# Kernel tuning notes

Measured on AMD Instinct MI355X. Metric: run time of the kernel, lower is better.

## Reference

```python
import jax, jax.numpy as jnp
import numpy as np

NUM_HEADS = 12


def _rel_indices(H, W):
    # [N, N, 3] with channels (dx, dy, dx^2+dy^2), N = H*W
    indx = jnp.arange(W)[None, :] - jnp.arange(W)[:, None]          # [W, W]
    indx = jnp.tile(indx, (H, H))                                    # [N, N]
    indy = jnp.arange(H)[None, :] - jnp.arange(H)[:, None]          # [H, H]
    indy = jnp.repeat(jnp.repeat(indy, W, axis=0), W, axis=1)        # [N, N]
    indd = indx ** 2 + indy ** 2
    return jnp.stack([indx, indy, indd], axis=-1).astype(jnp.float32)


def setup_inputs() -> dict:
    key = jax.random.key(0)
    ks = jax.random.split(key, 8)
    B, N, C = 16, 576, 768
    std = 0.02
    return {
        "x": jax.random.normal(ks[0], (B, N, C), dtype=jnp.float32),
        "Wq": jax.random.normal(ks[1], (C, C), dtype=jnp.float32) * std,
        "Wk": jax.random.normal(ks[2], (C, C), dtype=jnp.float32) * std,
        "Wv": jax.random.normal(ks[3], (C, C), dtype=jnp.float32) * std,
        "Wproj": jax.random.normal(ks[4], (C, C), dtype=jnp.float32) * std,
        "bproj": jnp.zeros((C,), dtype=jnp.float32),
        "pos_w": jax.random.normal(ks[5], (3, NUM_HEADS), dtype=jnp.float32) * std,
        "pos_b": jnp.zeros((NUM_HEADS,), dtype=jnp.float32),
        "gating": jnp.ones((NUM_HEADS,), dtype=jnp.float32),
        "H": 24,
        "W": 24,
    }


def reference(x, Wq, Wk, Wv, Wproj, bproj, pos_w, pos_b, gating, H, W):
    B, N, C = x.shape
    h = gating.shape[0]
    d = C // h
    scale = d ** (-0.5)

    def heads(t):  # [B,N,C] -> [B,h,N,d]
        return t.reshape(B, N, h, d).transpose(0, 2, 1, 3)

    q = heads(x @ Wq)
    k = heads(x @ Wk)
    v = heads(x @ Wv)

    # content scores: [B,h,N,N]
    patch_score = jax.nn.softmax(jnp.einsum('bhnd,bhmd->bhnm', q, k) * scale, axis=-1)

    # positional scores: shared across batch, [h,N,N]
    rel = _rel_indices(H, W)                      # [N,N,3]
    pos_score = jnp.einsum('nmc,ch->hnm', rel, pos_w) + pos_b[:, None, None]
    pos_score = jax.nn.softmax(pos_score, axis=-1)

    gate = jax.nn.sigmoid(gating)[None, :, None, None]  # [1,h,1,1]
    attn = (1.0 - gate) * patch_score + gate * pos_score[None]
    attn = attn / jnp.sum(attn, axis=-1, keepdims=True)

    out = jnp.einsum('bhnm,bhmd->bhnd', attn, v)         # [B,h,N,d]
    out = out.transpose(0, 2, 1, 3).reshape(B, N, C)
    return out @ Wproj + bproj
```

## Files before the change

### kernel.cpp

```cpp
#include <hip/hip_runtime.h>
#include <math.h>

#define B_ 16
#define N_ 576
#define C_ 768
#define NH 12
#define D_ 64
#define GW 24
#define STR 68
#define QKV 2304

typedef unsigned short u16;
typedef __bf16 bf16x8 __attribute__((ext_vector_type(8)));
typedef float f32x4 __attribute__((ext_vector_type(4)));

__device__ __forceinline__ u16 f2bf(float f) {
    unsigned u = __builtin_bit_cast(unsigned, f);
    unsigned r = (u + 0x7FFFu + ((u >> 16) & 1u)) >> 16;
    return (u16)r;
}
__device__ __forceinline__ float bf2f(u16 b) {
    unsigned u = ((unsigned)b) << 16;
    return __builtin_bit_cast(float, u);
}

__device__ __forceinline__ bf16x8 ldsF8u(const u16* p) {
    union { uint2 u[2]; bf16x8 v; } t;
    t.u[0] = *(const uint2*)p;
    t.u[1] = *(const uint2*)(p + 4);
    return t.v;
}
__device__ __forceinline__ bf16x8 ldsF8a(const u16* p) {
    union { uint4 u; bf16x8 v; } t;
    t.u = *(const uint4*)p;
    return t.v;
}

__device__ __forceinline__ void gload16(const u16* g, u16* l) {
    __builtin_amdgcn_global_load_lds(
        (const __attribute__((address_space(1))) void*)g,
        (__attribute__((address_space(3))) void*)l,
        16, 0, 0);
}

__global__ __launch_bounds__(256)
void prep_kernel(const float* __restrict__ x,
                 const float* __restrict__ w0, const float* __restrict__ w1,
                 const float* __restrict__ w2, const float* __restrict__ w3,
                 u16* __restrict__ xb, u16* __restrict__ wt_base)
{
    const int tid = threadIdx.x;
    if (blockIdx.z == 4) {
        const int flat = blockIdx.y * 24 + blockIdx.x;
#pragma unroll
        for (int it = 0; it < 12; ++it) {
            int idx = flat * 3072 + it * 256 + tid;
            float4 v = ((const float4*)x)[idx];
            u16 o[4] = {f2bf(v.x), f2bf(v.y), f2bf(v.z), f2bf(v.w)};
            *(uint2*)&xb[(size_t)idx * 4] = *(const uint2*)o;
        }
        return;
    }
    const float* srcs[4] = {w0, w1, w2, w3};
    const float* src = srcs[blockIdx.z];
    u16* dst = wt_base + (size_t)blockIdx.z * C_ * C_;
    __shared__ float t[32][33];
    const int bx = blockIdx.x * 32, by = blockIdx.y * 32;
    const int tx = tid & 31, ty = tid >> 5;
#pragma unroll
    for (int i = 0; i < 32; i += 8)
        t[ty + i][tx] = src[(size_t)(by + ty + i) * C_ + bx + tx];
    __syncthreads();
#pragma unroll
    for (int i = 0; i < 32; i += 8)
        dst[(size_t)(bx + ty + i) * C_ + by + tx] = f2bf(t[tx][ty + i]);
}

__global__ __launch_bounds__(256)
void mfma_gemm(const u16* __restrict__ A,
               const u16* __restrict__ BT,
               const float* __restrict__ bias,
               float* __restrict__ out,
               u16* __restrict__ outb,
               int ldo, int mode)
{
    const int K = C_;
    __shared__ __align__(16) u16 As[64 * 64];
    __shared__ __align__(16) u16 Bs[128 * 64];
    const int tid = threadIdx.x;
    const int wave = tid >> 6, lane = tid & 63;
    const int quad = lane >> 4, l16 = lane & 15;
    const int wy = wave >> 1, wx = wave & 1;
    const int tm = blockIdx.y * 64, tn = blockIdx.x * 128;

    const int lr = lane >> 3;
    const int sc = ((lane & 7) ^ lr) * 8;

    f32x4 acc[2][4];
#pragma unroll
    for (int i = 0; i < 2; ++i)
#pragma unroll
        for (int j = 0; j < 4; ++j)
            acc[i][j] = (f32x4){0.f, 0.f, 0.f, 0.f};

    for (int k0 = 0; k0 < K; k0 += 64) {
        __syncthreads();
#pragma unroll
        for (int t = 0; t < 2; ++t) {
            const int rg = wave * 16 + t * 8;
            gload16(A + (size_t)(tm + rg + lr) * K + k0 + sc, &As[rg * 64]);
        }
#pragma unroll
        for (int t = 0; t < 4; ++t) {
            const int rg = wave * 32 + t * 8;
            gload16(BT + (size_t)(tn + rg + lr) * K + k0 + sc, &Bs[rg * 64]);
        }
        __syncthreads();

#pragma unroll
        for (int kh = 0; kh < 2; ++kh) {
            const int s = (kh * 4 + quad) ^ (l16 & 7);
            bf16x8 aA[2], bB[4];
#pragma unroll
            for (int i = 0; i < 2; ++i)
                aA[i] = ldsF8a(&As[(wy * 32 + i * 16 + l16) * 64 + s * 8]);
#pragma unroll
            for (int j = 0; j < 4; ++j)
                bB[j] = ldsF8a(&Bs[(wx * 64 + j * 16 + l16) * 64 + s * 8]);
#pragma unroll
            for (int i = 0; i < 2; ++i)
#pragma unroll
                for (int j = 0; j < 4; ++j)
                    acc[i][j] = __builtin_amdgcn_mfma_f32_16x16x32_bf16(aA[i], bB[j], acc[i][j], 0, 0, 0);
        }
    }

    if (mode == 0) {
#pragma unroll
        for (int i = 0; i < 2; ++i) {
#pragma unroll
            for (int r = 0; r < 4; ++r) {
                const int m = tm + wy * 32 + i * 16 + quad * 4 + r;
#pragma unroll
                for (int j = 0; j < 4; ++j) {
                    const int c = tn + wx * 64 + j * 16 + l16;
                    out[(size_t)m * ldo + c] = acc[i][j][r] + bias[c];
                }
            }
        }
    } else {
        const float scale = (tn < C_) ? 0.125f : 1.0f;
#pragma unroll
        for (int i = 0; i < 2; ++i) {
#pragma unroll
            for (int r = 0; r < 4; ++r) {
                const int m = tm + wy * 32 + i * 16 + quad * 4 + r;
#pragma unroll
                for (int j = 0; j < 4; ++j) {
                    const int c = tn + wx * 64 + j * 16 + l16;
                    outb[(size_t)m * ldo + c] = f2bf(acc[i][j][r] * scale);
                }
            }
        }
    }
}

__global__ __launch_bounds__(256)
void tv_pos1_kernel(const u16* __restrict__ qkvb,
                    const float* __restrict__ pos_w,
                    u16* __restrict__ vtb,
                    float* __restrict__ T1)
{
    const int bh = blockIdx.y;
    const int b = bh / NH, h = bh % NH;
    const int tid = threadIdx.x;

    if (blockIdx.x < 9) {
        __shared__ u16 t[64 * 72];
        const int n0 = blockIdx.x * 64;
        const u16* src = qkvb + ((size_t)b * N_ + n0) * QKV + 2 * C_ + h * D_;
#pragma unroll
        for (int p = 0; p < 2; ++p) {
            int idx = p * 256 + tid;
            int r = idx >> 3, c = (idx & 7) << 3;
            *(uint4*)&t[r * 72 + c] = *(const uint4*)(src + (size_t)r * QKV + c);
        }
        __syncthreads();
        u16* dst = vtb + (size_t)bh * D_ * N_ + n0;
#pragma unroll
        for (int p = 0; p < 2; ++p) {
            int idx = p * 256 + tid;
            int dd = idx >> 3, n8 = (idx & 7) << 3;
            u16 o[8];
#pragma unroll
            for (int j = 0; j < 8; ++j) o[j] = t[(n8 + j) * 72 + dd];
            *(uint4*)(dst + (size_t)dd * N_ + n8) = *(const uint4*)o;
        }
        return;
    }

    __shared__ float ey[47];
    const float w1 = pos_w[NH + h], w2 = pos_w[2 * NH + h];
    if (tid < 47) {
        float dy = (float)(tid - 23);
        ey[tid] = __expf(w1 * dy + w2 * dy * dy);
    }
    __syncthreads();
    if (tid >= 192) return;
    const int mx = tid >> 3, c = (tid & 7) << 3;
    const u16* src = qkvb + (size_t)b * N_ * QKV + 2 * C_ + h * D_ + c;

#pragma unroll
    for (int np = 0; np < 3; ++np) {
        float acc[8][8];
#pragma unroll
        for (int q = 0; q < 8; ++q)
#pragma unroll
            for (int j = 0; j < 8; ++j) acc[q][j] = 0.f;
        for (int my = 0; my < GW; ++my) {
            union { uint4 u; u16 s[8]; } d;
            d.u = *(const uint4*)(src + (size_t)(my * GW + mx) * QKV);
            float vf[8];
#pragma unroll
            for (int j = 0; j < 8; ++j) vf[j] = bf2f(d.s[j]);
#pragma unroll
            for (int q = 0; q < 8; ++q) {
                float e = ey[my - (np * 8 + q) + 23];
#pragma unroll
                for (int j = 0; j < 8; ++j) acc[q][j] += e * vf[j];
            }
        }
#pragma unroll
        for (int q = 0; q < 8; ++q) {
            const int ny = np * 8 + q;
            float* dst = T1 + (((size_t)bh * GW + ny) * GW + mx) * D_ + c;
            *(float4*)dst       = *(float4*)&acc[q][0];
            *(float4*)(dst + 4) = *(float4*)&acc[q][4];
        }
    }
}

__global__ __launch_bounds__(256)
void pos_stage2_kernel(const float* __restrict__ T1,
                       const float* __restrict__ pos_w,
                       const float* __restrict__ gating,
                       u16* __restrict__ aob)
{
    const int bh = blockIdx.x;
    const int ny = blockIdx.y;
    const int b = bh / NH, h = bh % NH;
    const int tid = threadIdx.x;
    __shared__ float T1s[GW * D_];
    __shared__ float ex[47];
    __shared__ float SxA[GW];
    __shared__ float Sy;
    const float w0 = pos_w[h], w1 = pos_w[NH + h], w2 = pos_w[2 * NH + h];

    const float* tsrc = T1 + ((size_t)bh * GW + ny) * GW * D_;
#pragma unroll
    for (int i = 0; i < 2; ++i) {
        int idx = i * 256 + tid;
        if (idx < 384) ((float4*)T1s)[idx] = ((const float4*)tsrc)[idx];
    }
    if (tid < 47) {
        float dx = (float)(tid - 23);
        ex[tid] = __expf(w0 * dx + w2 * dx * dx);
    }
    if (tid == 192) {
        float s = 0.f;
        for (int my = 0; my < GW; ++my) {
            float dy = (float)(my - ny);
            s += __expf(w1 * dy + w2 * dy * dy);
        }
        Sy = s;
    }
    __syncthreads();
    if (tid < GW) {
        float s = 0.f;
        for (int mx = 0; mx < GW; ++mx) s += ex[mx - tid + 23];
        SxA[tid] = s;
    }
    __syncthreads();
    if (tid >= 192) return;
    const int nx = tid >> 3, c = (tid & 7) << 3;

    float acc[8];
#pragma unroll
    for (int j = 0; j < 8; ++j) acc[j] = 0.f;
    for (int mx = 0; mx < GW; ++mx) {
        float e = ex[mx - nx + 23];
        float4 t0 = *(float4*)&T1s[mx * D_ + c];
        float4 t1 = *(float4*)&T1s[mx * D_ + c + 4];
        acc[0] += e * t0.x; acc[1] += e * t0.y; acc[2] += e * t0.z; acc[3] += e * t0.w;
        acc[4] += e * t1.x; acc[5] += e * t1.y; acc[6] += e * t1.z; acc[7] += e * t1.w;
    }
    const float g = 1.f / (1.f + __expf(-gating[h]));
    const float sc = g / (SxA[nx] * Sy);
    const int n = ny * GW + nx;
    u16* dst = aob + ((size_t)b * N_ + n) * C_ + h * D_ + c;
    u16 cur[8];
    *(uint4*)cur = *(const uint4*)dst;
    u16 o[8];
#pragma unroll
    for (int j = 0; j < 8; ++j) o[j] = f2bf(bf2f(cur[j]) + sc * acc[j]);
    *(uint4*)dst = *(const uint4*)o;
}

__global__ __launch_bounds__(256)
void attn_kernel(const u16* __restrict__ qkvb,
                 const u16* __restrict__ vt,
                 const float* __restrict__ gating,
                 u16* __restrict__ ao)
{
    const int qt = blockIdx.x;
    const int bh = blockIdx.y;
    const int b = bh / NH, h = bh % NH;
    const int tid = threadIdx.x;
    const int wave = tid >> 6, lane = tid & 63;
    const int quad = lane >> 4, l16 = lane & 15;

    __shared__ u16 smem[3 * 64 * STR];
    u16* Kt = smem;
    u16* Vs = smem + 64 * STR;
    u16* Pb = smem + 2 * 64 * STR;

    const u16* qptr  = qkvb + ((size_t)b * N_ + qt * 64) * QKV + h * D_;
    const u16* kbase = qkvb + (size_t)b * N_ * QKV + C_ + h * D_;
    const u16* vbase = vt + (size_t)bh * D_ * N_;

    const int sr = tid >> 3;
    const int scol = (tid & 7) << 3;

#pragma unroll
    for (int p = 0; p < 2; ++p) {
        int r = p * 32 + sr;
        uint4 d = *(const uint4*)(qptr + (size_t)r * QKV + scol);
        *(uint2*)&Pb[r * STR + scol]     = make_uint2(d.x, d.y);
        *(uint2*)&Pb[r * STR + scol + 4] = make_uint2(d.z, d.w);
    }
    __syncthreads();

    const int arow = wave * 16 + l16;
    bf16x8 aq0 = ldsF8u(&Pb[arow * STR + quad * 8]);
    bf16x8 aq1 = ldsF8u(&Pb[arow * STR + 32 + quad * 8]);

    uint4 rk[2], rv[2];
    auto loadT = [&](int m0) {
#pragma unroll
        for (int p = 0; p < 2; ++p) {
            int r = p * 32 + sr;
            rk[p] = *(const uint4*)(kbase + (size_t)(m0 + r) * QKV + scol);
            rv[p] = *(const uint4*)(vbase + (size_t)r * N_ + m0 + scol);
        }
    };
    auto writeT = [&]() {
#pragma unroll
        for (int p = 0; p < 2; ++p) {
            int r = p * 32 + sr;
            *(uint2*)&Kt[r * STR + scol]     = make_uint2(rk[p].x, rk[p].y);
            *(uint2*)&Kt[r * STR + scol + 4] = make_uint2(rk[p].z, rk[p].w);
            *(uint2*)&Vs[r * STR + scol]     = make_uint2(rv[p].x, rv[p].y);
            *(uint2*)&Vs[r * STR + scol + 4] = make_uint2(rv[p].z, rv[p].w);
        }
    };

    loadT(0);

    f32x4 oc[4];
#pragma unroll
    for (int nt = 0; nt < 4; ++nt)
        oc[nt] = (f32x4){0.f, 0.f, 0.f, 0.f};
    float lrun[4] = {0.f, 0.f, 0.f, 0.f};

    for (int mt = 0; mt < 9; ++mt) {
        __syncthreads();
        writeT();
        __syncthreads();
        if (mt < 8) loadT((mt + 1) * 64);

        f32x4 s[4];
#pragma unroll
        for (int nt = 0; nt < 4; ++nt) {
            bf16x8 b0 = ldsF8u(&Kt[(nt * 16 + l16) * STR + quad * 8]);
            bf16x8 b1 = ldsF8u(&Kt[(nt * 16 + l16) * STR + 32 + quad * 8]);
            f32x4 z = (f32x4){0.f, 0.f, 0.f, 0.f};
            z = __builtin_amdgcn_mfma_f32_16x16x32_bf16(aq0, b0, z, 0, 0, 0);
            z = __builtin_amdgcn_mfma_f32_16x16x32_bf16(aq1, b1, z, 0, 0, 0);
            s[nt] = z;
        }

#pragma unroll
        for (int r = 0; r < 4; ++r) {
            const int prow = (wave * 16 + quad * 4 + r) * STR;
            float e0 = __expf(s[0][r]);
            float e1 = __expf(s[1][r]);
            float e2 = __expf(s[2][r]);
            float e3 = __expf(s[3][r]);
            Pb[prow +  0 + l16] = f2bf(e0);
            Pb[prow + 16 + l16] = f2bf(e1);
            Pb[prow + 32 + l16] = f2bf(e2);
            Pb[prow + 48 + l16] = f2bf(e3);
            lrun[r] += (e0 + e1) + (e2 + e3);
        }
        asm volatile("s_waitcnt lgkmcnt(0)" ::: "memory");

#pragma unroll
        for (int ks = 0; ks < 2; ++ks) {
            bf16x8 ap = ldsF8u(&Pb[arow * STR + ks * 32 + quad * 8]);
#pragma unroll
            for (int nt = 0; nt < 4; ++nt) {
                bf16x8 bv = ldsF8u(&Vs[(nt * 16 + l16) * STR + ks * 32 + quad * 8]);
                oc[nt] = __builtin_amdgcn_mfma_f32_16x16x32_bf16(ap, bv, oc[nt], 0, 0, 0);
            }
        }
    }

#pragma unroll
    for (int r = 0; r < 4; ++r) {
        lrun[r] += __shfl_xor(lrun[r], 1, 64);
        lrun[r] += __shfl_xor(lrun[r], 2, 64);
        lrun[r] += __shfl_xor(lrun[r], 4, 64);
        lrun[r] += __shfl_xor(lrun[r], 8, 64);
    }

    const float g = 1.f / (1.f + __expf(-gating[h]));
#pragma unroll
    for (int r = 0; r < 4; ++r) {
        const float sc = (1.f - g) / lrun[r];
        const int row = qt * 64 + wave * 16 + quad * 4 + r;
#pragma unroll
        for (int nt = 0; nt < 4; ++nt) {
            ao[((size_t)b * N_ + row) * C_ + h * D_ + nt * 16 + l16] =
                f2bf(oc[nt][r] * sc);
        }
    }
}

extern "C" void kernel_launch(void* const* d_in, const int* in_sizes, int n_in,
                              void* d_out, int out_size, void* d_ws, size_t ws_size,
                              hipStream_t stream)
{
    const float* x      = (const float*)d_in[0];
    const float* Wq     = (const float*)d_in[1];
    const float* Wk     = (const float*)d_in[2];
    const float* Wv     = (const float*)d_in[3];
    const float* Wproj  = (const float*)d_in[4];
    const float* bproj  = (const float*)d_in[5];
    const float* pos_w  = (const float*)d_in[6];
    const float* gating = (const float*)d_in[8];
    float* out = (float*)d_out;

    const size_t xe = (size_t)B_ * N_ * C_;
    const size_t we = (size_t)C_ * C_;
    const size_t qe = (size_t)B_ * N_ * QKV;
    u16* xb   = (u16*)d_ws;
    u16* wt   = xb + xe;
    u16* qkvb = wt + 4 * we;
    u16* vtb  = qkvb + qe;
    u16* aob  = vtb + xe;
    float* T1 = (float*)(aob + xe);
    size_t need = (size_t)(3 * xe + 4 * we + qe) * sizeof(u16)
                + (size_t)B_ * NH * GW * GW * D_ * sizeof(float);
    if (ws_size < need) return;

    prep_kernel<<<dim3(24, 24, 5), 256, 0, stream>>>(x, Wq, Wk, Wv, Wproj, xb, wt);

    mfma_gemm<<<dim3(18, 144), 256, 0, stream>>>(xb, wt, nullptr, nullptr,
                                                 qkvb, QKV, 1);
    tv_pos1_kernel<<<dim3(10, B_ * NH), 256, 0, stream>>>(qkvb, pos_w, vtb, T1);
    attn_kernel<<<dim3(9, B_ * NH), 256, 0, stream>>>(qkvb, vtb, gating, aob);
    pos_stage2_kernel<<<dim3(B_ * NH, GW), 256, 0, stream>>>(T1, pos_w, gating, aob);
    mfma_gemm<<<dim3(6, 144), 256, 0, stream>>>(aob, wt + 3 * we, bproj, out,
                                                nullptr, C_, 0);
}
```

Measured before the change: 261.0 us.

## Fuse V transpose into QKV GEMM epilogue and pos stage1 into attention

```diff
diff --git a/kernel.cpp b/kernel.cpp
--- a/kernel.cpp
+++ b/kernel.cpp
@@ -82,6 +82,7 @@
                const float* __restrict__ bias,
                float* __restrict__ out,
                u16* __restrict__ outb,
+               u16* __restrict__ vtb,
                int ldo, int mode)
 {
     const int K = C_;
@@ -162,80 +163,22 @@
                 }
             }
         }
-    }
-}
-
-__global__ __launch_bounds__(256)
-void tv_pos1_kernel(const u16* __restrict__ qkvb,
-                    const float* __restrict__ pos_w,
-                    u16* __restrict__ vtb,
-                    float* __restrict__ T1)
-{
-    const int bh = blockIdx.y;
-    const int b = bh / NH, h = bh % NH;
-    const int tid = threadIdx.x;
-
-    if (blockIdx.x < 9) {
-        __shared__ u16 t[64 * 72];
-        const int n0 = blockIdx.x * 64;
-        const u16* src = qkvb + ((size_t)b * N_ + n0) * QKV + 2 * C_ + h * D_;
-#pragma unroll
-        for (int p = 0; p < 2; ++p) {
-            int idx = p * 256 + tid;
-            int r = idx >> 3, c = (idx & 7) << 3;
-            *(uint4*)&t[r * 72 + c] = *(const uint4*)(src + (size_t)r * QKV + c);
-        }
-        __syncthreads();
-        u16* dst = vtb + (size_t)bh * D_ * N_ + n0;
-#pragma unroll
-        for (int p = 0; p < 2; ++p) {
-            int idx = p * 256 + tid;
-            int dd = idx >> 3, n8 = (idx & 7) << 3;
-            u16 o[8];
-#pragma unroll
-            for (int j = 0; j < 8; ++j) o[j] = t[(n8 + j) * 72 + dd];
-            *(uint4*)(dst + (size_t)dd * N_ + n8) = *(const uint4*)o;
-        }
-        return;
-    }
-
-    __shared__ float ey[47];
-    const float w1 = pos_w[NH + h], w2 = pos_w[2 * NH + h];
-    if (tid < 47) {
-        float dy = (float)(tid - 23);
-        ey[tid] = __expf(w1 * dy + w2 * dy * dy);
-    }
-    __syncthreads();
-    if (tid >= 192) return;
-    const int mx = tid >> 3, c = (tid & 7) << 3;
-    const u16* src = qkvb + (size_t)b * N_ * QKV + 2 * C_ + h * D_ + c;
-
-#pragma unroll
-    for (int np = 0; np < 3; ++np) {
-        float acc[8][8];
-#pragma unroll
-        for (int q = 0; q < 8; ++q)
-#pragma unroll
-            for (int j = 0; j < 8; ++j) acc[q][j] = 0.f;
-        for (int my = 0; my < GW; ++my) {
-            union { uint4 u; u16 s[8]; } d;
-            d.u = *(const uint4*)(src + (size_t)(my * GW + mx) * QKV);
-            float vf[8];
-#pragma unroll
-            for (int j = 0; j < 8; ++j) vf[j] = bf2f(d.s[j]);
-#pragma unroll
-            for (int q = 0; q < 8; ++q) {
-                float e = ey[my - (np * 8 + q) + 23];
-#pragma unroll
-                for (int j = 0; j < 8; ++j) acc[q][j] += e * vf[j];
-            }
-        }
-#pragma unroll
-        for (int q = 0; q < 8; ++q) {
-            const int ny = np * 8 + q;
-            float* dst = T1 + (((size_t)bh * GW + ny) * GW + mx) * D_ + c;
-            *(float4*)dst       = *(float4*)&acc[q][0];
-            *(float4*)(dst + 4) = *(float4*)&acc[q][4];
+        if (tn >= 2 * C_) {
+            const int b = tm / N_;
+#pragma unroll
+            for (int i = 0; i < 2; ++i) {
+                const int n0 = (tm % N_) + wy * 32 + i * 16 + quad * 4;
+#pragma unroll
+                for (int j = 0; j < 4; ++j) {
+                    const int cc = tn - 2 * C_ + wx * 64 + j * 16 + l16;
+                    const int hh = cc >> 6, dd = cc & 63;
+                    u16 o[4];
+#pragma unroll
+                    for (int r = 0; r < 4; ++r) o[r] = f2bf(acc[i][j][r]);
+                    *(uint2*)&vtb[(((size_t)b * NH + hh) * D_ + dd) * N_ + n0] =
+                        *(const uint2*)o;
+                }
+            }
         }
     }
 }
@@ -309,20 +252,65 @@
 __global__ __launch_bounds__(256)
 void attn_kernel(const u16* __restrict__ qkvb,
                  const u16* __restrict__ vt,
+                 const float* __restrict__ pos_w,
                  const float* __restrict__ gating,
-                 u16* __restrict__ ao)
+                 u16* __restrict__ ao,
+                 float* __restrict__ T1)
 {
     const int qt = blockIdx.x;
     const int bh = blockIdx.y;
     const int b = bh / NH, h = bh % NH;
     const int tid = threadIdx.x;
+
+    __shared__ __align__(16) u16 smem[2 * 64 * 64 + 64 * STR];
+
+    if (qt == 9) {
+        float* ey = (float*)smem;
+        const float w1 = pos_w[NH + h], w2 = pos_w[2 * NH + h];
+        if (tid < 47) {
+            float dy = (float)(tid - 23);
+            ey[tid] = __expf(w1 * dy + w2 * dy * dy);
+        }
+        __syncthreads();
+        if (tid >= 192) return;
+        const int mx = tid >> 3, c = (tid & 7) << 3;
+        const u16* src = qkvb + (size_t)b * N_ * QKV + 2 * C_ + h * D_ + c;
+#pragma unroll
+        for (int np = 0; np < 3; ++np) {
+            float acc[8][8];
+#pragma unroll
+            for (int q = 0; q < 8; ++q)
+#pragma unroll
+                for (int j = 0; j < 8; ++j) acc[q][j] = 0.f;
+            for (int my = 0; my < GW; ++my) {
+                union { uint4 u; u16 s[8]; } d;
+                d.u = *(const uint4*)(src + (size_t)(my * GW + mx) * QKV);
+                float vf[8];
+#pragma unroll
+                for (int j = 0; j < 8; ++j) vf[j] = bf2f(d.s[j]);
+#pragma unroll
+                for (int q = 0; q < 8; ++q) {
+                    float e = ey[my - (np * 8 + q) + 23];
+#pragma unroll
+                    for (int j = 0; j < 8; ++j) acc[q][j] += e * vf[j];
+                }
+            }
+#pragma unroll
+            for (int q = 0; q < 8; ++q) {
+                const int ny = np * 8 + q;
+                float* dst = T1 + (((size_t)bh * GW + ny) * GW + mx) * D_ + c;
+                *(float4*)dst       = *(float4*)&acc[q][0];
+                *(float4*)(dst + 4) = *(float4*)&acc[q][4];
+            }
+        }
+        return;
+    }
+
     const int wave = tid >> 6, lane = tid & 63;
     const int quad = lane >> 4, l16 = lane & 15;
-
-    __shared__ u16 smem[3 * 64 * STR];
     u16* Kt = smem;
-    u16* Vs = smem + 64 * STR;
-    u16* Pb = smem + 2 * 64 * STR;
+    u16* Vs = smem + 4096;
+    u16* Pb = smem + 8192;
 
     const u16* qptr  = qkvb + ((size_t)b * N_ + qt * 64) * QKV + h * D_;
     const u16* kbase = qkvb + (size_t)b * N_ * QKV + C_ + h * D_;
@@ -344,27 +332,9 @@
     bf16x8 aq0 = ldsF8u(&Pb[arow * STR + quad * 8]);
     bf16x8 aq1 = ldsF8u(&Pb[arow * STR + 32 + quad * 8]);
 
-    uint4 rk[2], rv[2];
-    auto loadT = [&](int m0) {
-#pragma unroll
-        for (int p = 0; p < 2; ++p) {
-            int r = p * 32 + sr;
-            rk[p] = *(const uint4*)(kbase + (size_t)(m0 + r) * QKV + scol);
-            rv[p] = *(const uint4*)(vbase + (size_t)r * N_ + m0 + scol);
-        }
-    };
-    auto writeT = [&]() {
-#pragma unroll
-        for (int p = 0; p < 2; ++p) {
-            int r = p * 32 + sr;
-            *(uint2*)&Kt[r * STR + scol]     = make_uint2(rk[p].x, rk[p].y);
-            *(uint2*)&Kt[r * STR + scol + 4] = make_uint2(rk[p].z, rk[p].w);
-            *(uint2*)&Vs[r * STR + scol]     = make_uint2(rv[p].x, rv[p].y);
-            *(uint2*)&Vs[r * STR + scol + 4] = make_uint2(rv[p].z, rv[p].w);
-        }
-    };
-
-    loadT(0);
+    const int lr = lane >> 3;
+    const int sg = ((lane & 7) ^ lr) * 8;
+    const int x7 = l16 & 7;
 
     f32x4 oc[4];
 #pragma unroll
@@ -373,16 +343,22 @@
     float lrun[4] = {0.f, 0.f, 0.f, 0.f};
 
     for (int mt = 0; mt < 9; ++mt) {
+        const int m0 = mt * 64;
         __syncthreads();
-        writeT();
+#pragma unroll
+        for (int t = 0; t < 2; ++t) {
+            const int rg = wave * 16 + t * 8;
+            gload16(kbase + (size_t)(m0 + rg + lr) * QKV + sg, &Kt[rg * 64]);
+            gload16(vbase + (size_t)(rg + lr) * N_ + m0 + sg, &Vs[rg * 64]);
+        }
         __syncthreads();
-        if (mt < 8) loadT((mt + 1) * 64);
 
         f32x4 s[4];
 #pragma unroll
         for (int nt = 0; nt < 4; ++nt) {
-            bf16x8 b0 = ldsF8u(&Kt[(nt * 16 + l16) * STR + quad * 8]);
-            bf16x8 b1 = ldsF8u(&Kt[(nt * 16 + l16) * STR + 32 + quad * 8]);
+            const int ro = (nt * 16 + l16) * 64;
+            bf16x8 b0 = ldsF8a(&Kt[ro + (quad ^ x7) * 8]);
+            bf16x8 b1 = ldsF8a(&Kt[ro + ((quad + 4) ^ x7) * 8]);
             f32x4 z = (f32x4){0.f, 0.f, 0.f, 0.f};
             z = __builtin_amdgcn_mfma_f32_16x16x32_bf16(aq0, b0, z, 0, 0, 0);
             z = __builtin_amdgcn_mfma_f32_16x16x32_bf16(aq1, b1, z, 0, 0, 0);
@@ -409,7 +385,8 @@
             bf16x8 ap = ldsF8u(&Pb[arow * STR + ks * 32 + quad * 8]);
 #pragma unroll
             for (int nt = 0; nt < 4; ++nt) {
-                bf16x8 bv = ldsF8u(&Vs[(nt * 16 + l16) * STR + ks * 32 + quad * 8]);
+                const int ro = (nt * 16 + l16) * 64;
+                bf16x8 bv = ldsF8a(&Vs[ro + ((ks * 4 + quad) ^ x7) * 8]);
                 oc[nt] = __builtin_amdgcn_mfma_f32_16x16x32_bf16(ap, bv, oc[nt], 0, 0, 0);
             }
         }
@@ -466,10 +443,10 @@
     prep_kernel<<<dim3(24, 24, 5), 256, 0, stream>>>(x, Wq, Wk, Wv, Wproj, xb, wt);
 
     mfma_gemm<<<dim3(18, 144), 256, 0, stream>>>(xb, wt, nullptr, nullptr,
-                                                 qkvb, QKV, 1);
-    tv_pos1_kernel<<<dim3(10, B_ * NH), 256, 0, stream>>>(qkvb, pos_w, vtb, T1);
-    attn_kernel<<<dim3(9, B_ * NH), 256, 0, stream>>>(qkvb, vtb, gating, aob);
+                                                 qkvb, vtb, QKV, 1);
+    attn_kernel<<<dim3(10, B_ * NH), 256, 0, stream>>>(qkvb, vtb, pos_w, gating,
+                                                       aob, T1);
     pos_stage2_kernel<<<dim3(B_ * NH, GW), 256, 0, stream>>>(T1, pos_w, gating, aob);
     mfma_gemm<<<dim3(6, 144), 256, 0, stream>>>(aob, wt + 3 * we, bproj, out,
-                                                nullptr, C_, 0);
-}
+                                                nullptr, nullptr, C_, 0);
+}
```

Result: faster. 248.9 us (-4.7%).
